# Performance work log

Hardware: AMD Instinct MI355X
Metric: run time of the kernel (lower is better)

## Reference

```python
import jax, jax.numpy as jnp
import numpy as np

THRESH = 0.9
NUM_HEADS = 4
HEAD_DIM = 8


def _ln(x, g, b, eps=1e-5):
    m = x.mean(-1, keepdims=True)
    v = ((x - m) ** 2).mean(-1, keepdims=True)
    return (x - m) * jax.lax.rsqrt(v + eps) * g + b


def setup_inputs() -> dict:
    key = jax.random.key(0)
    ks = jax.random.split(key, 32)
    n, d_in, h1, h2, d, ffn, nb = 4096, 512, 128, 64, 32, 64, 2

    def w(k, shape, fan_in):
        return jax.random.normal(k, shape, jnp.float32) * (1.0 / np.sqrt(fan_in))

    inp = {}
    inp["x"] = jax.random.normal(ks[0], (n, d_in), jnp.float32)
    # Autoencoder encoder: input_dim -> 128 -> 64 -> latent_dim
    inp["enc_w1"] = w(ks[1], (d_in, h1), d_in); inp["enc_b1"] = jnp.zeros((h1,), jnp.float32)
    inp["enc_w2"] = w(ks[2], (h1, h2), h1);     inp["enc_b2"] = jnp.zeros((h2,), jnp.float32)
    inp["enc_w3"] = w(ks[3], (h2, d), h2);      inp["enc_b3"] = jnp.zeros((d,), jnp.float32)
    # Transformer blocks (stacked over num_blocks=2)
    inp["wq"] = w(ks[4], (nb, d, d), d); inp["bq"] = jnp.zeros((nb, d), jnp.float32)
    inp["wk"] = w(ks[5], (nb, d, d), d); inp["bk"] = jnp.zeros((nb, d), jnp.float32)
    inp["wv"] = w(ks[6], (nb, d, d), d); inp["bv"] = jnp.zeros((nb, d), jnp.float32)
    inp["wo"] = w(ks[7], (nb, d, d), d); inp["bo"] = jnp.zeros((nb, d), jnp.float32)
    inp["ln1_g"] = jnp.ones((nb, d), jnp.float32);  inp["ln1_b"] = jnp.zeros((nb, d), jnp.float32)
    inp["ffn_w1"] = w(ks[8], (nb, d, ffn), d);      inp["ffn_b1"] = jnp.zeros((nb, ffn), jnp.float32)
    inp["ffn_w2"] = w(ks[9], (nb, ffn, d), ffn);    inp["ffn_b2"] = jnp.zeros((nb, d), jnp.float32)
    inp["ln2_g"] = jnp.ones((nb, d), jnp.float32);  inp["ln2_b"] = jnp.zeros((nb, d), jnp.float32)
    # Head: Linear(d,16) -> Tanh -> Linear(16, num_classes)
    inp["head_w1"] = w(ks[10], (d, 16), d);  inp["head_b1"] = jnp.zeros((16,), jnp.float32)
    inp["head_w2"] = w(ks[11], (16, 1), 16); inp["head_b2"] = jnp.zeros((1,), jnp.float32)
    return inp


def reference(x, enc_w1, enc_b1, enc_w2, enc_b2, enc_w3, enc_b3,
              wq, bq, wk, bk, wv, bv, wo, bo,
              ln1_g, ln1_b, ffn_w1, ffn_b1, ffn_w2, ffn_b2, ln2_g, ln2_b,
              head_w1, head_b1, head_w2, head_b2):
    # --- autoencoder encode: [n, d_in] -> [n, d] ---
    a = jax.nn.relu(x @ enc_w1 + enc_b1)
    a = jax.nn.relu(a @ enc_w2 + enc_b2)
    latent = a @ enc_w3 + enc_b3  # [n, d]

    # --- graph pool: cosine-sim threshold mask, per-node masked neighbor mean ---
    # self-similarity is 1.0 >= THRESH, so every node has >=1 neighbor (deg>=1)
    norms = jnp.linalg.norm(latent, axis=1, keepdims=True) + 1e-12
    normed = latent / norms
    sims = normed @ normed.T                                  # [n, n]
    mask = (sims >= THRESH).astype(latent.dtype)              # [n, n]
    deg = mask.sum(axis=1, keepdims=True)                     # [n, 1]
    pooled = latent + (mask @ latent) / deg                   # latent[i] + mean of neighbors

    # --- transformer blocks (post-LN, eval mode: dropout off) ---
    h = pooled[None]  # [1, n, d]
    n, d = pooled.shape
    nb = wq.shape[0]
    scale = 1.0 / np.sqrt(HEAD_DIM)
    for i in range(nb):
        q = (h @ wq[i] + bq[i]).reshape(1, n, NUM_HEADS, HEAD_DIM)
        k = (h @ wk[i] + bk[i]).reshape(1, n, NUM_HEADS, HEAD_DIM)
        v = (h @ wv[i] + bv[i]).reshape(1, n, NUM_HEADS, HEAD_DIM)
        scores = jnp.einsum('bqhd,bkhd->bhqk', q, k) * scale  # [1, H, n, n]
        attn = jax.nn.softmax(scores, axis=-1)
        o = jnp.einsum('bhqk,bkhd->bqhd', attn, v).reshape(1, n, d)
        o = o @ wo[i] + bo[i]
        h = _ln(h + o, ln1_g[i], ln1_b[i])
        f = jax.nn.relu(h @ ffn_w1[i] + ffn_b1[i]) @ ffn_w2[i] + ffn_b2[i]
        h = _ln(h + f, ln2_g[i], ln2_b[i])

    # --- head on mean-pooled sequence ---
    m = h.mean(axis=1)  # [1, d]
    out = jnp.tanh(m @ head_w1 + head_b1) @ head_w2 + head_b2  # [1, 1]
    return out.squeeze()
```

## Files before the change

### kernel.cpp

```cpp
#include <hip/hip_runtime.h>
#include <math.h>

#define N 4096
#define DIN 512
#define D 32
#define JC 8

__global__ __launch_bounds__(256) void enc_kernel(
    const float* __restrict__ x,
    const float* __restrict__ w1, const float* __restrict__ b1,
    const float* __restrict__ w2, const float* __restrict__ b2,
    const float* __restrict__ w3, const float* __restrict__ b3,
    float* __restrict__ latent, float* __restrict__ normed) {
  __shared__ float xs[8][512];
  __shared__ float h1s[8][128];
  __shared__ float h2s[8][64];
  __shared__ float w2s[128][64];
  __shared__ float w3s[64][32];
  const int t = threadIdx.x;
  const int r0 = blockIdx.x * 8;

  const float4* xg = (const float4*)(x + (size_t)r0 * DIN);
  float4* xl = (float4*)&xs[0][0];
#pragma unroll
  for (int i = 0; i < 4; ++i) xl[t + i * 256] = xg[t + i * 256];
  float4* w2l = (float4*)&w2s[0][0];
  const float4* w2g = (const float4*)w2;
#pragma unroll
  for (int i = 0; i < 8; ++i) w2l[t + i * 256] = w2g[t + i * 256];
  float4* w3l = (float4*)&w3s[0][0];
  const float4* w3g = (const float4*)w3;
#pragma unroll
  for (int i = 0; i < 2; ++i) w3l[t + i * 256] = w3g[t + i * 256];
  __syncthreads();

  {
    const int jc2 = (t & 63) * 2;
    const int rg = t >> 6;
    const int ra = rg * 2, rb = ra + 1;
    float a00 = b1[jc2], a01 = b1[jc2 + 1];
    float a10 = a00, a11 = a01;
    const float* wp = w1 + jc2;

#define ENC_LD4(P0, P1, P2, P3, KB)                         \
    P0 = *(const float2*)&wp[(size_t)(KB) * 128];           \
    P1 = *(const float2*)&wp[(size_t)((KB) + 1) * 128];     \
    P2 = *(const float2*)&wp[(size_t)((KB) + 2) * 128];     \
    P3 = *(const float2*)&wp[(size_t)((KB) + 3) * 128];

#define ENC_L1_STEP(W0, WA, WB, WC, KB)                               \
    {                                                                 \
      const float4 xa = *(const float4*)&xs[ra][KB];                  \
      const float4 xb = *(const float4*)&xs[rb][KB];                  \
      a00 = fmaf(xa.x, W0.x, a00);  a01 = fmaf(xa.x, W0.y, a01);      \
      a10 = fmaf(xb.x, W0.x, a10);  a11 = fmaf(xb.x, W0.y, a11);      \
      a00 = fmaf(xa.y, WA.x, a00);  a01 = fmaf(xa.y, WA.y, a01);      \
      a10 = fmaf(xb.y, WA.x, a10);  a11 = fmaf(xb.y, WA.y, a11);      \
      a00 = fmaf(xa.z, WB.x, a00);  a01 = fmaf(xa.z, WB.y, a01);      \
      a10 = fmaf(xb.z, WB.x, a10);  a11 = fmaf(xb.z, WB.y, a11);      \
      a00 = fmaf(xa.w, WC.x, a00);  a01 = fmaf(xa.w, WC.y, a01);      \
      a10 = fmaf(xb.w, WC.x, a10);  a11 = fmaf(xb.w, WC.y, a11);      \
    }

    float2 A0, A1, A2, A3, B0, B1, B2, B3, C0, C1, C2, C3, D0, D1, D2, D3;
    ENC_LD4(A0, A1, A2, A3, 0)
    ENC_LD4(B0, B1, B2, B3, 4)
    ENC_LD4(C0, C1, C2, C3, 8)
    ENC_LD4(D0, D1, D2, D3, 12)
    for (int k = 0; k < 512; k += 16) {
      ENC_L1_STEP(A0, A1, A2, A3, k + 0);
      if (k + 16 < 512) { ENC_LD4(A0, A1, A2, A3, k + 16) }
      ENC_L1_STEP(B0, B1, B2, B3, k + 4);
      if (k + 20 < 512) { ENC_LD4(B0, B1, B2, B3, k + 20) }
      ENC_L1_STEP(C0, C1, C2, C3, k + 8);
      if (k + 24 < 512) { ENC_LD4(C0, C1, C2, C3, k + 24) }
      ENC_L1_STEP(D0, D1, D2, D3, k + 12);
      if (k + 28 < 512) { ENC_LD4(D0, D1, D2, D3, k + 28) }
    }
#undef ENC_L1_STEP
#undef ENC_LD4
    h1s[ra][jc2] = fmaxf(a00, 0.f);
    h1s[ra][jc2 + 1] = fmaxf(a01, 0.f);
    h1s[rb][jc2] = fmaxf(a10, 0.f);
    h1s[rb][jc2 + 1] = fmaxf(a11, 0.f);
  }
  __syncthreads();

  {
    const int j = t & 63, rg = t >> 6;
    const int ra = rg * 2, rb = ra + 1;
    float a0 = b2[j], a1 = b2[j];
#pragma unroll 8
    for (int kk = 0; kk < 128; ++kk) {
      const float w = w2s[kk][j];
      a0 = fmaf(h1s[ra][kk], w, a0);
      a1 = fmaf(h1s[rb][kk], w, a1);
    }
    h2s[ra][j] = fmaxf(a0, 0.f);
    h2s[rb][j] = fmaxf(a1, 0.f);
  }
  __syncthreads();

  {
    const int j = t & 31, og = t >> 5;
    float acc = b3[j];
#pragma unroll 8
    for (int kk = 0; kk < 64; ++kk) acc = fmaf(h2s[og][kk], w3s[kk][j], acc);
    float s2 = acc * acc;
    s2 += __shfl_xor(s2, 1);
    s2 += __shfl_xor(s2, 2);
    s2 += __shfl_xor(s2, 4);
    s2 += __shfl_xor(s2, 8);
    s2 += __shfl_xor(s2, 16);
    const float inv = 1.0f / (sqrtf(s2) + 1e-12f);
    const size_t off = (size_t)(r0 + og) * D + j;
    latent[off] = acc;
    normed[off] = acc * inv;
  }
}

__global__ __launch_bounds__(256) void pool_kernel(const float* __restrict__ normed,
                                                   const float* __restrict__ latent,
                                                   float* __restrict__ pacc,
                                                   float* __restrict__ pdeg) {
  __shared__ float smem[8192 + 256];
  float* nt = smem;
  float* lt = smem + 4096;
  float* degr = smem + 8192;
  const int t = threadIdx.x;
  const int il = t & 63, g = t >> 6;
  const int i0 = blockIdx.x * 64;
  const int j0 = blockIdx.y * 512;

  float ni[32];
  const float* nrow = normed + (size_t)(i0 + il) * D;
#pragma unroll
  for (int c = 0; c < 32; ++c) ni[c] = nrow[c];

  float acc[32];
#pragma unroll
  for (int c = 0; c < 32; ++c) acc[c] = 0.f;
  float deg = 0.f;

  for (int jt = j0; jt < j0 + 512; jt += 128) {
    __syncthreads();
    const float4* ng = (const float4*)(normed + (size_t)jt * D);
    const float4* lg = (const float4*)(latent + (size_t)jt * D);
    float4* ntl = (float4*)nt;
    float4* ltl = (float4*)lt;
#pragma unroll
    for (int i = 0; i < 4; ++i) {
      ntl[t + i * 256] = ng[t + i * 256];
      ltl[t + i * 256] = lg[t + i * 256];
    }
    __syncthreads();
    for (int jj = g; jj < 128; jj += 4) {
      const float* nr = nt + jj * 32;
      float s = 0.f;
#pragma unroll
      for (int c = 0; c < 32; ++c) s = fmaf(ni[c], nr[c], s);
      if (s >= 0.9f) {
        deg += 1.f;
        const float* lrow = lt + jj * 32;
#pragma unroll
        for (int c = 0; c < 32; ++c) acc[c] += lrow[c];
      }
    }
  }
  __syncthreads();
  float* accr = smem;
#pragma unroll
  for (int c = 0; c < 32; ++c) accr[(g * 64 + il) * 32 + c] = acc[c];
  degr[t] = deg;
  __syncthreads();
  for (int e = t; e < 64 * 32; e += 256) {
    const float s = accr[e] + accr[2048 + e] + accr[4096 + e] + accr[6144 + e];
    pacc[((size_t)blockIdx.y * N + i0 + (e >> 5)) * 32 + (e & 31)] = s;
  }
  if (t < 64) {
    pdeg[(size_t)blockIdx.y * N + i0 + t] = degr[t] + degr[64 + t] + degr[128 + t] + degr[192 + t];
  }
}

__global__ __launch_bounds__(256) void pool_combine(const float* __restrict__ latent,
                                                    const float* __restrict__ pacc,
                                                    const float* __restrict__ pdeg,
                                                    float* __restrict__ h) {
  const int e = blockIdx.x * 256 + threadIdx.x;
  const int i = e >> 5;
  float s = 0.f, dg = 0.f;
#pragma unroll
  for (int gch = 0; gch < JC; ++gch) {
    s += pacc[(size_t)gch * N * 32 + e];
    dg += pdeg[(size_t)gch * N + i];
  }
  h[e] = latent[e] + s / dg;
}

__global__ __launch_bounds__(256) void qkv_kernel(
    const float* __restrict__ h,
    const float* __restrict__ wq, const float* __restrict__ bq,
    const float* __restrict__ wk, const float* __restrict__ bk,
    const float* __restrict__ wv, const float* __restrict__ bv,
    float* __restrict__ q, float* __restrict__ k, float* __restrict__ v,
    int* __restrict__ kmax2i) {
  __shared__ float hs[32][32];
  __shared__ float wsm[3][32][32];
  __shared__ int kred[4];
  const int t = threadIdx.x;
  const int r0 = blockIdx.x * 32;
  if (t < 4) kred[t] = 0;
  ((float4*)&hs[0][0])[t] = ((const float4*)(h + (size_t)r0 * 32))[t];
  ((float4*)&wsm[0][0][0])[t] = ((const float4*)wq)[t];
  ((float4*)&wsm[1][0][0])[t] = ((const float4*)wk)[t];
  ((float4*)&wsm[2][0][0])[t] = ((const float4*)wv)[t];
  __syncthreads();
  const int j = t & 31, og = t >> 5;
  const int head = j >> 3;
  float aq[4], ak[4], av[4];
#pragma unroll
  for (int u = 0; u < 4; ++u) { aq[u] = bq[j]; ak[u] = bk[j]; av[u] = bv[j]; }
  for (int kk = 0; kk < 32; ++kk) {
    const float wqv = wsm[0][kk][j], wkv = wsm[1][kk][j], wvv = wsm[2][kk][j];
#pragma unroll
    for (int u = 0; u < 4; ++u) {
      const float hh = hs[og * 4 + u][kk];
      aq[u] = fmaf(hh, wqv, aq[u]);
      ak[u] = fmaf(hh, wkv, ak[u]);
      av[u] = fmaf(hh, wvv, av[u]);
    }
  }
  const float scale = 1.4426950408889634f * 0.35355339059327373f;
#pragma unroll
  for (int u = 0; u < 4; ++u) {
    const size_t off = (size_t)(r0 + og * 4 + u) * 32 + j;
    q[off] = aq[u] * scale;
    k[off] = ak[u];
    v[off] = av[u];
  }
#pragma unroll
  for (int u = 0; u < 4; ++u) {
    float s2 = ak[u] * ak[u];
    s2 += __shfl_xor(s2, 1);
    s2 += __shfl_xor(s2, 2);
    s2 += __shfl_xor(s2, 4);
    if ((j & 7) == 0) atomicMax(&kred[head], __float_as_int(s2));
  }
  __syncthreads();
  if (t < 4) atomicMax(&kmax2i[t], kred[t]);
}

__global__ __launch_bounds__(256) __attribute__((amdgpu_waves_per_eu(2, 2)))
void attn_kernel(const float* __restrict__ q,
                 const float* __restrict__ k,
                 const float* __restrict__ v,
                 const int* __restrict__ kmax2i,
                 float* __restrict__ apacc,
                 float* __restrict__ apl) {
  __shared__ float4 tiles[1024];
  float4* kls = tiles;
  float4* vls = tiles + 512;
  const int t = threadIdx.x;
  const int jg = t & 7, head = (t >> 3) & 3, rg = t >> 5;
  const int r0 = blockIdx.x * 64;
  const int j0 = blockIdx.y * (N / JC);

  const float km2 = __int_as_float(kmax2i[head]);

  float4 qa[8], qb[8], accA[8], accB[8];
  float mneg[8], l[8];
#pragma unroll
  for (int u = 0; u < 8; ++u) {
    const float* qr = q + (size_t)(r0 + rg * 8 + u) * 32 + head * 8;
    qa[u] = ((const float4*)qr)[0];
    qb[u] = ((const float4*)qr)[1];
    const float qn2 = qa[u].x * qa[u].x + qa[u].y * qa[u].y + qa[u].z * qa[u].z + qa[u].w * qa[u].w +
                      qb[u].x * qb[u].x + qb[u].y * qb[u].y + qb[u].z * qb[u].z + qb[u].w * qb[u].w;
    mneg[u] = -sqrtf(qn2 * km2);
    l[u] = 0.f;
    accA[u] = make_float4(0.f, 0.f, 0.f, 0.f);
    accB[u] = make_float4(0.f, 0.f, 0.f, 0.f);
  }

  const int h2 = head * 2;
  const int s0 = h2 ^ jg, s1 = (h2 + 1) ^ jg;
  for (int jt = j0; jt < j0 + (N / JC); jt += 64) {
    __syncthreads();
    const float4* kg = (const float4*)(k + (size_t)jt * 32);
    const float4* vg = (const float4*)(v + (size_t)jt * 32);
#pragma unroll
    for (int i = 0; i < 2; ++i) {
      const int gidx = t + i * 256;
      const int r = gidx >> 3, cc = gidx & 7, slot = cc ^ (r & 7);
      kls[r * 8 + slot] = kg[gidx];
      vls[r * 8 + slot] = vg[gidx];
    }
    __syncthreads();
#pragma unroll 2
    for (int it = 0; it < 8; ++it) {
      const int jj = it * 8 + jg;
      const float4 ka = kls[jj * 8 + s0];
      const float4 kb = kls[jj * 8 + s1];
      const float4 va = vls[jj * 8 + s0];
      const float4 vb = vls[jj * 8 + s1];
#pragma unroll
      for (int u = 0; u < 8; ++u) {
        float s = fmaf(qa[u].x, ka.x, mneg[u]);
        s = fmaf(qa[u].y, ka.y, s);
        s = fmaf(qa[u].z, ka.z, s);
        s = fmaf(qa[u].w, ka.w, s);
        s = fmaf(qb[u].x, kb.x, s);
        s = fmaf(qb[u].y, kb.y, s);
        s = fmaf(qb[u].z, kb.z, s);
        s = fmaf(qb[u].w, kb.w, s);
        const float p = __builtin_amdgcn_exp2f(s);
        l[u] += p;
        accA[u].x = fmaf(p, va.x, accA[u].x);
        accA[u].y = fmaf(p, va.y, accA[u].y);
        accA[u].z = fmaf(p, va.z, accA[u].z);
        accA[u].w = fmaf(p, va.w, accA[u].w);
        accB[u].x = fmaf(p, vb.x, accB[u].x);
        accB[u].y = fmaf(p, vb.y, accB[u].y);
        accB[u].z = fmaf(p, vb.z, accB[u].z);
        accB[u].w = fmaf(p, vb.w, accB[u].w);
      }
    }
  }
#pragma unroll
  for (int u = 0; u < 8; ++u) {
#pragma unroll
    for (int m = 1; m <= 4; m <<= 1) {
      accA[u].x += __shfl_xor(accA[u].x, m);
      accA[u].y += __shfl_xor(accA[u].y, m);
      accA[u].z += __shfl_xor(accA[u].z, m);
      accA[u].w += __shfl_xor(accA[u].w, m);
      accB[u].x += __shfl_xor(accB[u].x, m);
      accB[u].y += __shfl_xor(accB[u].y, m);
      accB[u].z += __shfl_xor(accB[u].z, m);
      accB[u].w += __shfl_xor(accB[u].w, m);
      l[u] += __shfl_xor(l[u], m);
    }
  }
  if (jg == 0) {
#pragma unroll
    for (int u = 0; u < 8; ++u) {
      const int row = r0 + rg * 8 + u;
      float* ap = apacc + (size_t)blockIdx.y * N * 32 + (size_t)row * 32 + head * 8;
      ((float4*)ap)[0] = accA[u];
      ((float4*)ap)[1] = accB[u];
      apl[(size_t)blockIdx.y * N * 4 + (size_t)row * 4 + head] = l[u];
    }
  }
}

__global__ __launch_bounds__(256) void acombine(const float* __restrict__ apacc,
                                                const float* __restrict__ apl,
                                                float* __restrict__ attno) {
  const int e = blockIdx.x * 256 + threadIdx.x;
  const int row = e >> 5;
  const int hh = (e >> 3) & 3;
  float L = 0.f, S = 0.f;
#pragma unroll
  for (int jc = 0; jc < JC; ++jc) {
    L += apl[(size_t)jc * N * 4 + row * 4 + hh];
    S += apacc[(size_t)jc * N * 32 + e];
  }
  attno[e] = S / L;
}

__global__ __launch_bounds__(256) void oln1_kernel(const float* __restrict__ attno,
                                                   const float* __restrict__ wo,
                                                   const float* __restrict__ bo,
                                                   const float* __restrict__ g,
                                                   const float* __restrict__ b,
                                                   float* __restrict__ h) {
  __shared__ float als[32][32];
  __shared__ float wols[32][32];
  __shared__ float ys[32][33];
  const int t = threadIdx.x;
  const int r0 = blockIdx.x * 32;
  ((float4*)&als[0][0])[t] = ((const float4*)(attno + (size_t)r0 * 32))[t];
  ((float4*)&wols[0][0])[t] = ((const float4*)wo)[t];
  __syncthreads();
  const int j = t & 31, og = t >> 5;
  float acc[4];
#pragma unroll
  for (int u = 0; u < 4; ++u) acc[u] = bo[j];
  for (int kk = 0; kk < 32; ++kk) {
    const float w = wols[kk][j];
#pragma unroll
    for (int u = 0; u < 4; ++u) acc[u] = fmaf(als[og * 4 + u][kk], w, acc[u]);
  }
#pragma unroll
  for (int u = 0; u < 4; ++u) {
    const int r = og * 4 + u;
    ys[r][j] = h[(size_t)(r0 + r) * 32 + j] + acc[u];
  }
  __syncthreads();
  if (t < 32) {
    float mu = 0.f;
#pragma unroll
    for (int c = 0; c < 32; ++c) mu += ys[t][c];
    mu *= (1.f / 32.f);
    float var = 0.f;
#pragma unroll
    for (int c = 0; c < 32; ++c) {
      const float dd = ys[t][c] - mu;
      var = fmaf(dd, dd, var);
    }
    var *= (1.f / 32.f);
    const float rs = rsqrtf(var + 1e-5f);
#pragma unroll
    for (int c = 0; c < 32; ++c)
      h[(size_t)(r0 + t) * 32 + c] = (ys[t][c] - mu) * rs * g[c] + b[c];
  }
}

__global__ __launch_bounds__(256) void ffn_kernel(const float* __restrict__ hin,
                                                  const float* __restrict__ w1,
                                                  const float* __restrict__ b1,
                                                  const float* __restrict__ w2,
                                                  const float* __restrict__ b2,
                                                  const float* __restrict__ g,
                                                  const float* __restrict__ bb,
                                                  float* __restrict__ h) {
  __shared__ float hs[32][32];
  __shared__ float w1s[32][64];
  __shared__ float w2s[64][32];
  __shared__ float mids[32][64];
  __shared__ float ys[32][33];
  const int t = threadIdx.x;
  const int r0 = blockIdx.x * 32;
  ((float4*)&hs[0][0])[t] = ((const float4*)(hin + (size_t)r0 * 32))[t];
#pragma unroll
  for (int i = 0; i < 2; ++i) {
    ((float4*)&w1s[0][0])[t + i * 256] = ((const float4*)w1)[t + i * 256];
    ((float4*)&w2s[0][0])[t + i * 256] = ((const float4*)w2)[t + i * 256];
  }
  __syncthreads();
  {
    const int jm = t & 63, gg = t >> 6;
    float acc[8];
#pragma unroll
    for (int u = 0; u < 8; ++u) acc[u] = b1[jm];
    for (int kk = 0; kk < 32; ++kk) {
      const float w = w1s[kk][jm];
#pragma unroll
      for (int u = 0; u < 8; ++u) acc[u] = fmaf(hs[gg * 8 + u][kk], w, acc[u]);
    }
#pragma unroll
    for (int u = 0; u < 8; ++u) mids[gg * 8 + u][jm] = fmaxf(acc[u], 0.f);
  }
  __syncthreads();
  {
    const int j = t & 31, og = t >> 5;
    float acc[4];
#pragma unroll
    for (int u = 0; u < 4; ++u) acc[u] = b2[j];
    for (int kk = 0; kk < 64; ++kk) {
      const float w = w2s[kk][j];
#pragma unroll
      for (int u = 0; u < 4; ++u) acc[u] = fmaf(mids[og * 4 + u][kk], w, acc[u]);
    }
#pragma unroll
    for (int u = 0; u < 4; ++u) {
      const int r = og * 4 + u;
      ys[r][j] = hs[r][j] + acc[u];
    }
  }
  __syncthreads();
  if (t < 32) {
    float mu = 0.f;
#pragma unroll
    for (int c = 0; c < 32; ++c) mu += ys[t][c];
    mu *= (1.f / 32.f);
    float var = 0.f;
#pragma unroll
    for (int c = 0; c < 32; ++c) {
      const float dd = ys[t][c] - mu;
      var = fmaf(dd, dd, var);
    }
    var *= (1.f / 32.f);
    const float rs = rsqrtf(var + 1e-5f);
#pragma unroll
    for (int c = 0; c < 32; ++c)
      h[(size_t)(r0 + t) * 32 + c] = (ys[t][c] - mu) * rs * g[c] + bb[c];
  }
}

__global__ __launch_bounds__(256) void headp_kernel(const float* __restrict__ h,
                                                    float* __restrict__ partial) {
  __shared__ float red[8][32];
  const int t = threadIdx.x;
  const int c = t & 31, rg = t >> 5;
  const int r0 = blockIdx.x * 64;
  float s = 0.f;
#pragma unroll
  for (int u = 0; u < 8; ++u) s += h[(size_t)(r0 + rg * 8 + u) * 32 + c];
  red[rg][c] = s;
  __syncthreads();
  if (t < 32) {
    float ss = 0.f;
#pragma unroll
    for (int u = 0; u < 8; ++u) ss += red[u][t];
    partial[blockIdx.x * 32 + t] = ss;
  }
}

__global__ __launch_bounds__(64) void headf_kernel(const float* __restrict__ partial,
                                                   const float* __restrict__ w1,
                                                   const float* __restrict__ b1,
                                                   const float* __restrict__ w2,
                                                   const float* __restrict__ b2,
                                                   float* __restrict__ out) {
  __shared__ float mls[32];
  __shared__ float tls[16];
  const int t = threadIdx.x;
  if (t < 32) {
    float s = 0.f;
    for (int bb = 0; bb < 64; ++bb) s += partial[bb * 32 + t];
    mls[t] = s * (1.f / 4096.f);
  }
  __syncthreads();
  if (t < 16) {
    float a = b1[t];
#pragma unroll
    for (int c = 0; c < 32; ++c) a = fmaf(mls[c], w1[c * 16 + t], a);
    tls[t] = tanhf(a);
  }
  __syncthreads();
  if (t == 0) {
    float o = b2[0];
#pragma unroll
    for (int jj = 0; jj < 16; ++jj) o = fmaf(tls[jj], w2[jj], o);
    out[0] = o;
  }
}

extern "C" void kernel_launch(void* const* d_in, const int* in_sizes, int n_in,
                              void* d_out, int out_size, void* d_ws, size_t ws_size,
                              hipStream_t stream) {
  const float* x      = (const float*)d_in[0];
  const float* enc_w1 = (const float*)d_in[1];
  const float* enc_b1 = (const float*)d_in[2];
  const float* enc_w2 = (const float*)d_in[3];
  const float* enc_b2 = (const float*)d_in[4];
  const float* enc_w3 = (const float*)d_in[5];
  const float* enc_b3 = (const float*)d_in[6];
  const float* wq     = (const float*)d_in[7];
  const float* bq     = (const float*)d_in[8];
  const float* wk     = (const float*)d_in[9];
  const float* bk     = (const float*)d_in[10];
  const float* wv     = (const float*)d_in[11];
  const float* bv     = (const float*)d_in[12];
  const float* wo     = (const float*)d_in[13];
  const float* bo     = (const float*)d_in[14];
  const float* ln1_g  = (const float*)d_in[15];
  const float* ln1_b  = (const float*)d_in[16];
  const float* ffn_w1 = (const float*)d_in[17];
  const float* ffn_b1 = (const float*)d_in[18];
  const float* ffn_w2 = (const float*)d_in[19];
  const float* ffn_b2 = (const float*)d_in[20];
  const float* ln2_g  = (const float*)d_in[21];
  const float* ln2_b  = (const float*)d_in[22];
  const float* head_w1 = (const float*)d_in[23];
  const float* head_b1 = (const float*)d_in[24];
  const float* head_w2 = (const float*)d_in[25];
  const float* head_b2 = (const float*)d_in[26];

  float* ws      = (float*)d_ws;
  float* latent  = ws;
  float* normed  = ws + 131072;
  float* h       = ws + 262144;
  float* q       = ws + 393216;
  float* k       = ws + 524288;
  float* v       = ws + 655360;
  float* attno   = ws + 786432;
  float* shreg   = ws + 917504;
  float* p_acc   = shreg;
  float* p_deg   = shreg + 1048576;
  float* a_acc   = shreg;
  float* a_l     = shreg + 1048576;
  int*   kmax2i  = (int*)(ws + 2097152);
  float* partial = ws + 2097216;

  hipMemsetAsync(kmax2i, 0, 8 * sizeof(int), stream);

  enc_kernel<<<512, 256, 0, stream>>>(x, enc_w1, enc_b1, enc_w2, enc_b2, enc_w3, enc_b3,
                                      latent, normed);
  pool_kernel<<<dim3(64, JC), 256, 0, stream>>>(normed, latent, p_acc, p_deg);
  pool_combine<<<512, 256, 0, stream>>>(latent, p_acc, p_deg, h);

  for (int blk = 0; blk < 2; ++blk) {
    qkv_kernel<<<128, 256, 0, stream>>>(h, wq + blk * 1024, bq + blk * 32,
                                        wk + blk * 1024, bk + blk * 32,
                                        wv + blk * 1024, bv + blk * 32, q, k, v,
                                        kmax2i + blk * 4);
    attn_kernel<<<dim3(64, JC), 256, 0, stream>>>(q, k, v, kmax2i + blk * 4, a_acc, a_l);
    acombine<<<512, 256, 0, stream>>>(a_acc, a_l, attno);
    oln1_kernel<<<128, 256, 0, stream>>>(attno, wo + blk * 1024, bo + blk * 32,
                                         ln1_g + blk * 32, ln1_b + blk * 32, h);
    ffn_kernel<<<128, 256, 0, stream>>>(h, ffn_w1 + blk * 2048, ffn_b1 + blk * 64,
                                        ffn_w2 + blk * 2048, ffn_b2 + blk * 32,
                                        ln2_g + blk * 32, ln2_b + blk * 32, h);
  }

  headp_kernel<<<64, 256, 0, stream>>>(h, partial);
  headf_kernel<<<1, 64, 0, stream>>>(partial, head_w1, head_b1, head_w2, head_b2, (float*)d_out);
}
```

Measured before the change: 199.9 us.

## Split-K encoder layer-1 across warps and prefetch next K/V tile into registers

The first encoder layer now gives each 64-thread group a quarter of the 512-wide reduction for all 8 rows. Each w1 element loaded from global memory is reused across 8 rows instead of 2, and the partial sums are reduced through shared memory before bias and ReLU. Separately, the attention kernel prefetches the next K/V tile into registers while computing on the current tile, overlapping global loads with compute. The cost is an extra 16KB of shared memory, an extra barrier, and more registers, which may lower occupancy.

```diff
diff --git a/kernel.cpp b/kernel.cpp
--- a/kernel.cpp
+++ b/kernel.cpp
@@ -13,6 +13,7 @@
     const float* __restrict__ w3, const float* __restrict__ b3,
     float* __restrict__ latent, float* __restrict__ normed) {
   __shared__ float xs[8][512];
+  __shared__ float h1p[4][8][128];
   __shared__ float h1s[8][128];
   __shared__ float h2s[8][64];
   __shared__ float w2s[128][64];
@@ -36,30 +37,29 @@
 
   {
     const int jc2 = (t & 63) * 2;
-    const int rg = t >> 6;
-    const int ra = rg * 2, rb = ra + 1;
-    float a00 = b1[jc2], a01 = b1[jc2 + 1];
-    float a10 = a00, a11 = a01;
-    const float* wp = w1 + jc2;
-
-#define ENC_LD4(P0, P1, P2, P3, KB)                         \
-    P0 = *(const float2*)&wp[(size_t)(KB) * 128];           \
-    P1 = *(const float2*)&wp[(size_t)((KB) + 1) * 128];     \
-    P2 = *(const float2*)&wp[(size_t)((KB) + 2) * 128];     \
-    P3 = *(const float2*)&wp[(size_t)((KB) + 3) * 128];
-
-#define ENC_L1_STEP(W0, WA, WB, WC, KB)                               \
-    {                                                                 \
-      const float4 xa = *(const float4*)&xs[ra][KB];                  \
-      const float4 xb = *(const float4*)&xs[rb][KB];                  \
-      a00 = fmaf(xa.x, W0.x, a00);  a01 = fmaf(xa.x, W0.y, a01);      \
-      a10 = fmaf(xb.x, W0.x, a10);  a11 = fmaf(xb.x, W0.y, a11);      \
-      a00 = fmaf(xa.y, WA.x, a00);  a01 = fmaf(xa.y, WA.y, a01);      \
-      a10 = fmaf(xb.y, WA.x, a10);  a11 = fmaf(xb.y, WA.y, a11);      \
-      a00 = fmaf(xa.z, WB.x, a00);  a01 = fmaf(xa.z, WB.y, a01);      \
-      a10 = fmaf(xb.z, WB.x, a10);  a11 = fmaf(xb.z, WB.y, a11);      \
-      a00 = fmaf(xa.w, WC.x, a00);  a01 = fmaf(xa.w, WC.y, a01);      \
-      a10 = fmaf(xb.w, WC.x, a10);  a11 = fmaf(xb.w, WC.y, a11);      \
+    const int kq = t >> 6;
+    const int kb = kq * 128;
+    float a0[8], a1[8];
+#pragma unroll
+    for (int r = 0; r < 8; ++r) { a0[r] = 0.f; a1[r] = 0.f; }
+    const float* wp = w1 + (size_t)kb * 128 + jc2;
+
+#define ENC_LD4(P0, P1, P2, P3, KK)                          \
+    P0 = *(const float2*)&wp[(size_t)(KK) * 128];            \
+    P1 = *(const float2*)&wp[(size_t)((KK) + 1) * 128];      \
+    P2 = *(const float2*)&wp[(size_t)((KK) + 2) * 128];      \
+    P3 = *(const float2*)&wp[(size_t)((KK) + 3) * 128];
+
+#define ENC_STEP(W0, WA, WB, WC, KK)                                   \
+    {                                                                  \
+      _Pragma("unroll")                                                \
+      for (int r = 0; r < 8; ++r) {                                    \
+        const float4 xv = *(const float4*)&xs[r][kb + (KK)];           \
+        a0[r] = fmaf(xv.x, W0.x, a0[r]); a1[r] = fmaf(xv.x, W0.y, a1[r]); \
+        a0[r] = fmaf(xv.y, WA.x, a0[r]); a1[r] = fmaf(xv.y, WA.y, a1[r]); \
+        a0[r] = fmaf(xv.z, WB.x, a0[r]); a1[r] = fmaf(xv.z, WB.y, a1[r]); \
+        a0[r] = fmaf(xv.w, WC.x, a0[r]); a1[r] = fmaf(xv.w, WC.y, a1[r]); \
+      }                                                                \
     }
 
     float2 A0, A1, A2, A3, B0, B1, B2, B3, C0, C1, C2, C3, D0, D1, D2, D3;
@@ -67,22 +67,32 @@
     ENC_LD4(B0, B1, B2, B3, 4)
     ENC_LD4(C0, C1, C2, C3, 8)
     ENC_LD4(D0, D1, D2, D3, 12)
-    for (int k = 0; k < 512; k += 16) {
-      ENC_L1_STEP(A0, A1, A2, A3, k + 0);
-      if (k + 16 < 512) { ENC_LD4(A0, A1, A2, A3, k + 16) }
-      ENC_L1_STEP(B0, B1, B2, B3, k + 4);
-      if (k + 20 < 512) { ENC_LD4(B0, B1, B2, B3, k + 20) }
-      ENC_L1_STEP(C0, C1, C2, C3, k + 8);
-      if (k + 24 < 512) { ENC_LD4(C0, C1, C2, C3, k + 24) }
-      ENC_L1_STEP(D0, D1, D2, D3, k + 12);
-      if (k + 28 < 512) { ENC_LD4(D0, D1, D2, D3, k + 28) }
-    }
-#undef ENC_L1_STEP
+    for (int kk = 0; kk < 128; kk += 16) {
+      ENC_STEP(A0, A1, A2, A3, kk + 0);
+      if (kk + 16 < 128) { ENC_LD4(A0, A1, A2, A3, kk + 16) }
+      ENC_STEP(B0, B1, B2, B3, kk + 4);
+      if (kk + 20 < 128) { ENC_LD4(B0, B1, B2, B3, kk + 20) }
+      ENC_STEP(C0, C1, C2, C3, kk + 8);
+      if (kk + 24 < 128) { ENC_LD4(C0, C1, C2, C3, kk + 24) }
+      ENC_STEP(D0, D1, D2, D3, kk + 12);
+      if (kk + 28 < 128) { ENC_LD4(D0, D1, D2, D3, kk + 28) }
+    }
+#undef ENC_STEP
 #undef ENC_LD4
-    h1s[ra][jc2] = fmaxf(a00, 0.f);
-    h1s[ra][jc2 + 1] = fmaxf(a01, 0.f);
-    h1s[rb][jc2] = fmaxf(a10, 0.f);
-    h1s[rb][jc2 + 1] = fmaxf(a11, 0.f);
+#pragma unroll
+    for (int r = 0; r < 8; ++r) {
+      h1p[kq][r][jc2] = a0[r];
+      h1p[kq][r][jc2 + 1] = a1[r];
+    }
+  }
+  __syncthreads();
+
+#pragma unroll
+  for (int e0 = 0; e0 < 1024; e0 += 256) {
+    const int e = e0 + t;
+    const int r = e >> 7, c = e & 127;
+    const float s = b1[c] + ((h1p[0][r][c] + h1p[1][r][c]) + (h1p[2][r][c] + h1p[3][r][c]));
+    h1s[r][c] = fmaxf(s, 0.f);
   }
   __syncthreads();
 
@@ -282,20 +292,33 @@
     accB[u] = make_float4(0.f, 0.f, 0.f, 0.f);
   }
 
+  float4 kr0, kr1, vr0, vr1;
+  {
+    const float4* kg = (const float4*)(k + (size_t)j0 * 32);
+    const float4* vg = (const float4*)(v + (size_t)j0 * 32);
+    kr0 = kg[t]; kr1 = kg[t + 256];
+    vr0 = vg[t]; vr1 = vg[t + 256];
+  }
+
+  const int rA = t >> 3, slotA = (t & 7) ^ (rA & 7);
+  const int g1 = t + 256;
+  const int rB = g1 >> 3, slotB = (g1 & 7) ^ (rB & 7);
+
   const int h2 = head * 2;
   const int s0 = h2 ^ jg, s1 = (h2 + 1) ^ jg;
   for (int jt = j0; jt < j0 + (N / JC); jt += 64) {
     __syncthreads();
-    const float4* kg = (const float4*)(k + (size_t)jt * 32);
-    const float4* vg = (const float4*)(v + (size_t)jt * 32);
-#pragma unroll
-    for (int i = 0; i < 2; ++i) {
-      const int gidx = t + i * 256;
-      const int r = gidx >> 3, cc = gidx & 7, slot = cc ^ (r & 7);
-      kls[r * 8 + slot] = kg[gidx];
-      vls[r * 8 + slot] = vg[gidx];
-    }
+    kls[rA * 8 + slotA] = kr0;
+    kls[rB * 8 + slotB] = kr1;
+    vls[rA * 8 + slotA] = vr0;
+    vls[rB * 8 + slotB] = vr1;
     __syncthreads();
+    if (jt + 64 < j0 + (N / JC)) {
+      const float4* kg = (const float4*)(k + (size_t)(jt + 64) * 32);
+      const float4* vg = (const float4*)(v + (size_t)(jt + 64) * 32);
+      kr0 = kg[t]; kr1 = kg[t + 256];
+      vr0 = vg[t]; vr1 = vg[t + 256];
+    }
 #pragma unroll 2
     for (int it = 0; it < 8; ++it) {
       const int jj = it * 8 + jg;
```

New measurement: 180.6 us. 9.6% less time.
